# Kernel tuning notes

Measured on AMD Instinct MI355X. Metric: run time of the kernel, lower is better.

## Reference

```python
import jax, jax.numpy as jnp
import numpy as np

B, C, D, H, K = 512, 112, 128, 8, 8  # batch, channels(=seq), d_model, heads, conv kernel
HD = D // H
SCALE = HD ** -0.5
BN_EPS = 1e-5
LN_EPS = 1e-5


def setup_inputs() -> dict:
    key = jax.random.key(0)
    ks = jax.random.split(key, 12)
    s = 0.05
    return {
        "x": jax.random.normal(ks[0], (B, C, D), jnp.float32),
        "conv_w": jax.random.normal(ks[1], (C, 1, K), jnp.float32) * s,
        "conv_b": jax.random.normal(ks[2], (C,), jnp.float32) * s,
        "bn_g": jnp.ones((C,), jnp.float32),
        "bn_b": jnp.zeros((C,), jnp.float32),
        "bn_m": jnp.zeros((C,), jnp.float32),
        "bn_v": jnp.ones((C,), jnp.float32),
        "wq": jax.random.normal(ks[3], (D, D), jnp.float32) * s,
        "bq": jax.random.normal(ks[4], (D,), jnp.float32) * s,
        "wk": jax.random.normal(ks[5], (D, D), jnp.float32) * s,
        "bk": jax.random.normal(ks[6], (D,), jnp.float32) * s,
        "wv": jax.random.normal(ks[7], (D, D), jnp.float32) * s,
        "bv": jax.random.normal(ks[8], (D,), jnp.float32) * s,
        "wo": jax.random.normal(ks[9], (D, D), jnp.float32) * s,
        "bo": jax.random.normal(ks[10], (D,), jnp.float32) * s,
        "ln_g": jnp.ones((D,), jnp.float32),
        "ln_b": jnp.zeros((D,), jnp.float32),
    }


def _forward(x, conv_w, conv_b, bn_g, bn_b, bn_m, bn_v,
             wq, bq, wk, bk, wv, bv, wo, bo, ln_g, ln_b):
    # resnet_1: depthwise Conv1d(padding='same', k=8) -> GELU -> BatchNorm1d (eval)
    # torch 'same' padding for even k: left = (k-1)//2 = 3, right = 4
    h = jax.lax.conv_general_dilated(
        x, conv_w, window_strides=(1,), padding=[(3, 4)],
        dimension_numbers=("NCH", "OIH", "NCH"), feature_group_count=C)
    h = h + conv_b[None, :, None]
    h = jax.nn.gelu(h, approximate=False)
    h = (h - bn_m[None, :, None]) * (bn_g[None, :, None] * jax.lax.rsqrt(bn_v + BN_EPS)[None, :, None]) + bn_b[None, :, None]
    src = x + h  # [B, C, D]; attention treats C as sequence dim

    # multi-head attention (hand-rolled, res_attention path with prev=None)
    q = (src @ wq.T + bq).reshape(B, C, H, HD).transpose(0, 2, 1, 3)  # [B,H,S,hd]
    k = (src @ wk.T + bk).reshape(B, C, H, HD).transpose(0, 2, 1, 3)
    v = (src @ wv.T + bv).reshape(B, C, H, HD).transpose(0, 2, 1, 3)
    scores = jnp.einsum("bhqd,bhkd->bhqk", q, k) * SCALE  # [B,H,S,S]
    attn = jax.nn.softmax(scores, axis=-1)
    out = jnp.einsum("bhqk,bhkd->bhqd", attn, v)  # [B,H,S,hd]
    out = out.transpose(0, 2, 1, 3).reshape(B, C, D)
    out = out @ wo.T + bo

    # residual + LayerNorm over last dim
    src = src + out
    mu = jnp.mean(src, axis=-1, keepdims=True)
    var = jnp.mean(jnp.square(src - mu), axis=-1, keepdims=True)
    src = (src - mu) * jax.lax.rsqrt(var + LN_EPS) * ln_g + ln_b
    return src


def reference(x, conv_w, conv_b, bn_g, bn_b, bn_m, bn_v,
              wq, bq, wk, bk, wv, bv, wo, bo, ln_g, ln_b):
    return _forward(x, conv_w, conv_b, bn_g, bn_b, bn_m, bn_v,
                    wq, bq, wk, bk, wv, bv, wo, bo, ln_g, ln_b)
```

## Files before the change

### kernel.cpp

```cpp
#include <hip/hip_runtime.h>
#include <hip/hip_bf16.h>

#define BB 512
#define CC 112
#define DD 128
#define HH 8
#define HD 16
#define KK 8

typedef unsigned short u16;
typedef short short8 __attribute__((ext_vector_type(8)));
typedef float f32x4 __attribute__((ext_vector_type(4)));

#define MFMA16(a, b, c) __builtin_amdgcn_mfma_f32_16x16x32_bf16(a, b, c, 0, 0, 0)

#define PAD 140

__device__ inline u16 f2bf(float f) {
  union { float f; unsigned u; } v{f};
  unsigned r = (v.u + 0x7FFFu + ((v.u >> 16) & 1u)) >> 16;
  return (u16)r;
}

__global__ __launch_bounds__(128) void k_conv(
    const float* __restrict__ x, const float* __restrict__ cw,
    const float* __restrict__ cb, const float* __restrict__ bg,
    const float* __restrict__ bb_, const float* __restrict__ bm,
    const float* __restrict__ bv, float* __restrict__ src,
    u16* __restrict__ src_b,
    const float* __restrict__ wq, const float* __restrict__ wk,
    const float* __restrict__ wv, const float* __restrict__ wo,
    u16* __restrict__ w_b) {
  const int row = blockIdx.x;
  const int c = row % CC;
  const int d = threadIdx.x;
  __shared__ float sx[DD];
  const size_t base = (size_t)row * DD;
  const float xv = x[base + d];
  sx[d] = xv;
  if (row < 512) {
    const int i = row * 128 + d;
    const int sel = i >> 14, off = i & 16383;
    const float* ws4 = (sel == 0) ? wq : (sel == 1) ? wk : (sel == 2) ? wv : wo;
    w_b[i] = f2bf(ws4[off]);
  }
  __syncthreads();
  float acc = 0.f;
#pragma unroll
  for (int k = 0; k < KK; ++k) {
    const int j = d - 3 + k;
    const float xn = (j >= 0 && j < DD) ? sx[j] : 0.f;
    acc = fmaf(xn, cw[c * KK + k], acc);
  }
  acc += cb[c];
  const float g = 0.5f * acc * (1.f + erff(acc * 0.70710678118654752440f));
  const float h = (g - bm[c]) * (bg[c] * rsqrtf(bv[c] + 1e-5f)) + bb_[c];
  const float s = xv + h;
  src[base + d] = s;
  src_b[base + d] = f2bf(s);
}

__global__ __launch_bounds__(256) void k_qkv(
    const u16* __restrict__ src_b, const u16* __restrict__ w_b,
    const float* __restrict__ bq, const float* __restrict__ bk,
    const float* __restrict__ bv,
    u16* __restrict__ qb, u16* __restrict__ kb, u16* __restrict__ vb) {
  __shared__ u16 sw[128 * PAD];
  const int t = threadIdx.x;
  const int wave = t >> 6, lane = t & 63;
  const int quad = lane >> 4, n = lane & 15;
  const int row0 = blockIdx.x * 64 + wave * 16;

  short8 A[4];
  {
    const size_t rbase = (size_t)(row0 + n) * DD;
#pragma unroll
    for (int kf = 0; kf < 4; ++kf)
      A[kf] = *(const short8*)(src_b + rbase + kf * 32 + quad * 8);
  }
  size_t base_r[4];
#pragma unroll
  for (int r = 0; r < 4; ++r) {
    const int g = row0 + quad * 4 + r;
    const int b_ = g / CC, c_ = g - b_ * CC;
    base_r[r] = ((size_t)b_ * HH * CC + c_) * HD + n;
  }

  const float* const biases[3] = {bq, bk, bv};
  u16* const outs[3] = {qb, kb, vb};
  for (int m = 0; m < 3; ++m) {
    __syncthreads();
    {
      const uint4* wsrc = (const uint4*)(w_b + m * 16384);
      for (int i = t; i < 2048; i += 256) {
        const int r = i >> 4, c = i & 15;
        *(uint4*)&sw[r * PAD + c * 8] = wsrc[r * 16 + c];
      }
    }
    __syncthreads();
    const float* __restrict__ bias = biases[m];
    u16* __restrict__ o = outs[m];
#pragma unroll
    for (int nt = 0; nt < 8; ++nt) {
      f32x4 acc = {0.f, 0.f, 0.f, 0.f};
#pragma unroll
      for (int kf = 0; kf < 4; ++kf) {
        const short8 Bf =
            *(const short8*)&sw[(nt * 16 + n) * PAD + kf * 32 + quad * 8];
        acc = MFMA16(A[kf], Bf, acc);
      }
      const float bcol = bias[nt * 16 + n];
      const size_t hoff = (size_t)nt * CC * HD;
#pragma unroll
      for (int r = 0; r < 4; ++r)
        o[base_r[r] + hoff] = f2bf(acc[r] + bcol);
    }
  }
}

__global__ __launch_bounds__(448) void k_attn(
    const u16* __restrict__ qb_, const u16* __restrict__ kb_,
    const u16* __restrict__ vb_, u16* __restrict__ ab_) {
  const int bh = blockIdx.x;
  const int b = bh >> 3, h = bh & 7;
  const int t = threadIdx.x;
  const int wave = t >> 6;
  const int lane = t & 63;
  const int quad = lane >> 4, n = lane & 15;
  __shared__ u16 VT[HD * PAD];
  __shared__ u16 PL[7 * 16 * PAD];
  const u16* __restrict__ qh = qb_ + (size_t)bh * CC * HD;
  const u16* __restrict__ kh = kb_ + (size_t)bh * CC * HD;
  const u16* __restrict__ vh = vb_ + (size_t)bh * CC * HD;
  u16* __restrict__ aout = ab_ + (size_t)b * CC * DD + h * HD;

  for (int i = t; i < HD * 128; i += 448) {
    const int c = i >> 4, e = i & 15;
    VT[e * PAD + c] = (c < CC) ? vh[c * HD + e] : (u16)0;
  }
  u16* __restrict__ PW = PL + wave * 16 * PAD;
  for (int i = lane; i < 256; i += 64)
    PW[(i >> 4) * PAD + 112 + (i & 15)] = 0;
  __syncthreads();

  const int mt = wave;
  short8 Aq = {};
  if (quad < 2)
    Aq = *(const short8*)(qh + (size_t)(mt * 16 + n) * HD + quad * 8);
  float s[7][4];
#pragma unroll
  for (int jt = 0; jt < 7; ++jt) {
    short8 Bk = {};
    if (quad < 2)
      Bk = *(const short8*)(kh + (size_t)(jt * 16 + n) * HD + quad * 8);
    f32x4 acc = {0.f, 0.f, 0.f, 0.f};
    acc = MFMA16(Aq, Bk, acc);
#pragma unroll
    for (int r = 0; r < 4; ++r) s[jt][r] = acc[r] * 0.25f;
  }
  float mx[4];
#pragma unroll
  for (int r = 0; r < 4; ++r) {
    float m = s[0][r];
#pragma unroll
    for (int jt = 1; jt < 7; ++jt) m = fmaxf(m, s[jt][r]);
    mx[r] = m;
  }
#pragma unroll
  for (int d = 1; d < 16; d <<= 1)
#pragma unroll
    for (int r = 0; r < 4; ++r) mx[r] = fmaxf(mx[r], __shfl_xor(mx[r], d));
  float sm[4] = {0.f, 0.f, 0.f, 0.f};
#pragma unroll
  for (int jt = 0; jt < 7; ++jt)
#pragma unroll
    for (int r = 0; r < 4; ++r) {
      const float p = __expf(s[jt][r] - mx[r]);
      sm[r] += p;
      PW[(quad * 4 + r) * PAD + jt * 16 + n] = f2bf(p);
    }
#pragma unroll
  for (int d = 1; d < 16; d <<= 1)
#pragma unroll
    for (int r = 0; r < 4; ++r) sm[r] += __shfl_xor(sm[r], d);
  __threadfence_block();
  f32x4 o = {0.f, 0.f, 0.f, 0.f};
#pragma unroll
  for (int f = 0; f < 4; ++f) {
    const short8 Ap = *(const short8*)&PW[n * PAD + f * 32 + quad * 8];
    const short8 Bv = *(const short8*)&VT[n * PAD + f * 32 + quad * 8];
    o = MFMA16(Ap, Bv, o);
  }
#pragma unroll
  for (int r = 0; r < 4; ++r) {
    const float val = o[r] * (1.f / sm[r]);
    aout[(size_t)(mt * 16 + quad * 4 + r) * DD + n] = f2bf(val);
  }
}

__global__ __launch_bounds__(256) void k_out(
    const u16* __restrict__ a_b, const u16* __restrict__ w_bo,
    const float* __restrict__ bo, const float* __restrict__ src,
    const float* __restrict__ lg, const float* __restrict__ lb,
    float* __restrict__ out) {
  __shared__ u16 sw[128 * PAD];
  const int t = threadIdx.x;
  const int wave = t >> 6, lane = t & 63;
  const int quad = lane >> 4, n = lane & 15;
  const int row0 = blockIdx.x * 64 + wave * 16;
  {
    const uint4* wsrc = (const uint4*)w_bo;
    for (int i = t; i < 2048; i += 256) {
      const int r = i >> 4, c = i & 15;
      *(uint4*)&sw[r * PAD + c * 8] = wsrc[r * 16 + c];
    }
  }
  short8 A[4];
  {
    const size_t rbase = (size_t)(row0 + n) * DD;
#pragma unroll
    for (int kf = 0; kf < 4; ++kf)
      A[kf] = *(const short8*)(a_b + rbase + kf * 32 + quad * 8);
  }
  __syncthreads();
  float v[8][4];
#pragma unroll
  for (int nt = 0; nt < 8; ++nt) {
    f32x4 acc = {0.f, 0.f, 0.f, 0.f};
#pragma unroll
    for (int kf = 0; kf < 4; ++kf) {
      const short8 Bf =
          *(const short8*)&sw[(nt * 16 + n) * PAD + kf * 32 + quad * 8];
      acc = MFMA16(A[kf], Bf, acc);
    }
    const int col = nt * 16 + n;
    const float bcol = bo[col];
#pragma unroll
    for (int r = 0; r < 4; ++r)
      v[nt][r] = acc[r] + bcol + src[(size_t)(row0 + quad * 4 + r) * DD + col];
  }
  float sum[4] = {0.f, 0.f, 0.f, 0.f}, sq[4] = {0.f, 0.f, 0.f, 0.f};
#pragma unroll
  for (int nt = 0; nt < 8; ++nt)
#pragma unroll
    for (int r = 0; r < 4; ++r) {
      sum[r] += v[nt][r];
      sq[r] = fmaf(v[nt][r], v[nt][r], sq[r]);
    }
#pragma unroll
  for (int d = 1; d < 16; d <<= 1)
#pragma unroll
    for (int r = 0; r < 4; ++r) {
      sum[r] += __shfl_xor(sum[r], d);
      sq[r] += __shfl_xor(sq[r], d);
    }
  float mu[4], rs[4];
#pragma unroll
  for (int r = 0; r < 4; ++r) {
    mu[r] = sum[r] * (1.f / DD);
    const float var = sq[r] * (1.f / DD) - mu[r] * mu[r];
    rs[r] = rsqrtf(var + 1e-5f);
  }
#pragma unroll
  for (int nt = 0; nt < 8; ++nt) {
    const int col = nt * 16 + n;
    const float g = lg[col], be = lb[col];
#pragma unroll
    for (int r = 0; r < 4; ++r)
      out[(size_t)(row0 + quad * 4 + r) * DD + col] =
          (v[nt][r] - mu[r]) * rs[r] * g + be;
  }
}

extern "C" void kernel_launch(void* const* d_in, const int* in_sizes, int n_in,
                              void* d_out, int out_size, void* d_ws,
                              size_t ws_size, hipStream_t stream) {
  (void)in_sizes; (void)n_in; (void)out_size; (void)ws_size;
  const float* x   = (const float*)d_in[0];
  const float* cw  = (const float*)d_in[1];
  const float* cb  = (const float*)d_in[2];
  const float* bg  = (const float*)d_in[3];
  const float* bb  = (const float*)d_in[4];
  const float* bm  = (const float*)d_in[5];
  const float* bv  = (const float*)d_in[6];
  const float* wq  = (const float*)d_in[7];
  const float* bq  = (const float*)d_in[8];
  const float* wk  = (const float*)d_in[9];
  const float* bk  = (const float*)d_in[10];
  const float* wv  = (const float*)d_in[11];
  const float* bvv = (const float*)d_in[12];
  const float* wo  = (const float*)d_in[13];
  const float* bo  = (const float*)d_in[14];
  const float* lg  = (const float*)d_in[15];
  const float* lb  = (const float*)d_in[16];
  float* out = (float*)d_out;

  const size_t NE = (size_t)BB * CC * DD;
  float* s_src = (float*)d_ws;
  u16* ub = (u16*)((char*)d_ws + NE * 4);
  u16* src_b = ub;
  u16* q_b   = ub + NE;
  u16* k_b   = ub + 2 * NE;
  u16* v_b   = ub + 3 * NE;
  u16* a_b   = ub + 4 * NE;
  u16* w_b   = ub + 5 * NE;

  k_conv<<<BB * CC, 128, 0, stream>>>(x, cw, cb, bg, bb, bm, bv, s_src, src_b,
                                      wq, wk, wv, wo, w_b);
  k_qkv<<<(BB * CC) / 64, 256, 0, stream>>>(src_b, w_b, bq, bk, bvv,
                                            q_b, k_b, v_b);
  k_attn<<<BB * HH, 448, 0, stream>>>(q_b, k_b, v_b, a_b);
  k_out<<<(BB * CC) / 64, 256, 0, stream>>>(a_b, w_b + 3 * 16384, bo, s_src,
                                            lg, lb, out);
}
```

Measured before the change: 196.2 us.

## Fuse conv into QKV projection, use 32x32 MFMA attention, drop fp32 src buffer

Merges the depthwise conv/GELU/BN kernel into the QKV projection kernel, computing src directly in registers from x and converting weights to bf16 on the fly. This removes one launch and the fp32 src round trip. V is now written pre-transposed, and attention is rebuilt around 32x32x16 MFMA with 4 waves, exp2-based softmax, and normalization folded into P before the PV product. The output kernel reads the bf16 src for the residual, which lowers residual precision.

```diff
diff --git a/kernel.cpp b/kernel.cpp
--- a/kernel.cpp
+++ b/kernel.cpp
@@ -11,95 +11,113 @@
 typedef unsigned short u16;
 typedef short short8 __attribute__((ext_vector_type(8)));
 typedef float f32x4 __attribute__((ext_vector_type(4)));
+typedef float f32x16 __attribute__((ext_vector_type(16)));
 
 #define MFMA16(a, b, c) __builtin_amdgcn_mfma_f32_16x16x32_bf16(a, b, c, 0, 0, 0)
-
-#define PAD 140
+#define MFMA32(a, b, c) __builtin_amdgcn_mfma_f32_32x32x16_bf16(a, b, c, 0, 0, 0)
+
+#define PAD 136
 
 __device__ inline u16 f2bf(float f) {
   union { float f; unsigned u; } v{f};
   unsigned r = (v.u + 0x7FFFu + ((v.u >> 16) & 1u)) >> 16;
   return (u16)r;
 }
-
-__global__ __launch_bounds__(128) void k_conv(
+__device__ inline float bf2f(u16 u) {
+  union { unsigned u; float f; } v;
+  v.u = ((unsigned)u) << 16;
+  return v.f;
+}
+__device__ inline unsigned pk2(float a, float b) {
+  __hip_bfloat162 h = __float22bfloat162_rn(float2{a, b});
+  union { __hip_bfloat162 h; unsigned u; } v{h};
+  return v.u;
+}
+
+__global__ __launch_bounds__(256) void k_cqkv(
     const float* __restrict__ x, const float* __restrict__ cw,
     const float* __restrict__ cb, const float* __restrict__ bg,
     const float* __restrict__ bb_, const float* __restrict__ bm,
-    const float* __restrict__ bv, float* __restrict__ src,
-    u16* __restrict__ src_b,
-    const float* __restrict__ wq, const float* __restrict__ wk,
-    const float* __restrict__ wv, const float* __restrict__ wo,
-    u16* __restrict__ w_b) {
-  const int row = blockIdx.x;
-  const int c = row % CC;
-  const int d = threadIdx.x;
-  __shared__ float sx[DD];
-  const size_t base = (size_t)row * DD;
-  const float xv = x[base + d];
-  sx[d] = xv;
-  if (row < 512) {
-    const int i = row * 128 + d;
-    const int sel = i >> 14, off = i & 16383;
-    const float* ws4 = (sel == 0) ? wq : (sel == 1) ? wk : (sel == 2) ? wv : wo;
-    w_b[i] = f2bf(ws4[off]);
-  }
-  __syncthreads();
-  float acc = 0.f;
-#pragma unroll
-  for (int k = 0; k < KK; ++k) {
-    const int j = d - 3 + k;
-    const float xn = (j >= 0 && j < DD) ? sx[j] : 0.f;
-    acc = fmaf(xn, cw[c * KK + k], acc);
-  }
-  acc += cb[c];
-  const float g = 0.5f * acc * (1.f + erff(acc * 0.70710678118654752440f));
-  const float h = (g - bm[c]) * (bg[c] * rsqrtf(bv[c] + 1e-5f)) + bb_[c];
-  const float s = xv + h;
-  src[base + d] = s;
-  src_b[base + d] = f2bf(s);
-}
-
-__global__ __launch_bounds__(256) void k_qkv(
-    const u16* __restrict__ src_b, const u16* __restrict__ w_b,
-    const float* __restrict__ bq, const float* __restrict__ bk,
     const float* __restrict__ bv,
-    u16* __restrict__ qb, u16* __restrict__ kb, u16* __restrict__ vb) {
+    const float* __restrict__ wq, const float* __restrict__ bq,
+    const float* __restrict__ wk, const float* __restrict__ bk,
+    const float* __restrict__ wv, const float* __restrict__ bvv,
+    u16* __restrict__ src_b, u16* __restrict__ qb, u16* __restrict__ kb,
+    u16* __restrict__ vtb) {
   __shared__ u16 sw[128 * PAD];
   const int t = threadIdx.x;
   const int wave = t >> 6, lane = t & 63;
   const int quad = lane >> 4, n = lane & 15;
-  const int row0 = blockIdx.x * 64 + wave * 16;
+  const int row_g = blockIdx.x * 64 + wave * 16 + n;
+  const int ch = row_g % CC;
+
+  const float4 w0 = *(const float4*)(cw + ch * KK);
+  const float4 w1 = *(const float4*)(cw + ch * KK + 4);
+  const float cbv = cb[ch];
+  const float bscale = bg[ch] * rsqrtf(bv[ch] + 1e-5f);
+  const float bmv = bm[ch], bbv = bb_[ch];
+
+  const float* __restrict__ xr = x + (size_t)row_g * DD;
+  u16* __restrict__ sbr = src_b + (size_t)row_g * DD;
 
   short8 A[4];
-  {
-    const size_t rbase = (size_t)(row0 + n) * DD;
-#pragma unroll
-    for (int kf = 0; kf < 4; ++kf)
-      A[kf] = *(const short8*)(src_b + rbase + kf * 32 + quad * 8);
-  }
-  size_t base_r[4];
+#pragma unroll
+  for (int kf = 0; kf < 4; ++kf) {
+    const int c0 = kf * 32 + quad * 8;
+    float in[16];
+#pragma unroll
+    for (int f = 0; f < 4; ++f) {
+      const int fi = (c0 >> 2) - 1 + f;
+      float4 vv = {0.f, 0.f, 0.f, 0.f};
+      if (fi >= 0 && fi < 32) vv = ((const float4*)xr)[fi];
+      in[f * 4 + 0] = vv.x; in[f * 4 + 1] = vv.y;
+      in[f * 4 + 2] = vv.z; in[f * 4 + 3] = vv.w;
+    }
+    u16 ob[8];
+#pragma unroll
+    for (int i = 0; i < 8; ++i) {
+      float a = 0.f;
+      a = fmaf(in[i + 1], w0.x, a);
+      a = fmaf(in[i + 2], w0.y, a);
+      a = fmaf(in[i + 3], w0.z, a);
+      a = fmaf(in[i + 4], w0.w, a);
+      a = fmaf(in[i + 5], w1.x, a);
+      a = fmaf(in[i + 6], w1.y, a);
+      a = fmaf(in[i + 7], w1.z, a);
+      a = fmaf(in[i + 8], w1.w, a);
+      a += cbv;
+      const float g = 0.5f * a * (1.f + erff(a * 0.70710678118654752440f));
+      const float s = in[i + 4] + (g - bmv) * bscale + bbv;
+      ob[i] = f2bf(s);
+    }
+    A[kf] = *(short8*)ob;
+    *(short8*)(sbr + c0) = A[kf];
+  }
+
+  const int row0w = blockIdx.x * 64 + wave * 16;
+  int qk_base[4], vt_base[4];
 #pragma unroll
   for (int r = 0; r < 4; ++r) {
-    const int g = row0 + quad * 4 + r;
+    const int g = row0w + quad * 4 + r;
     const int b_ = g / CC, c_ = g - b_ * CC;
-    base_r[r] = ((size_t)b_ * HH * CC + c_) * HD + n;
-  }
-
-  const float* const biases[3] = {bq, bk, bv};
-  u16* const outs[3] = {qb, kb, vb};
+    qk_base[r] = (b_ * (HH * CC) + c_) * HD + n;
+    vt_base[r] = b_ * (HH * HD * CC) + n * CC + c_;
+  }
+
+  const float* const wmats[3] = {wq, wk, wv};
+  const float* const biases[3] = {bq, bk, bvv};
   for (int m = 0; m < 3; ++m) {
     __syncthreads();
     {
-      const uint4* wsrc = (const uint4*)(w_b + m * 16384);
-      for (int i = t; i < 2048; i += 256) {
-        const int r = i >> 4, c = i & 15;
-        *(uint4*)&sw[r * PAD + c * 8] = wsrc[r * 16 + c];
+      const float4* wsrc = (const float4*)wmats[m];
+      for (int i = t; i < 4096; i += 256) {
+        const int r = i >> 5, c4 = (i & 31) * 4;
+        const float4 vv = wsrc[i];
+        *(uint2*)&sw[r * PAD + c4] = uint2{pk2(vv.x, vv.y), pk2(vv.z, vv.w)};
       }
     }
     __syncthreads();
     const float* __restrict__ bias = biases[m];
-    u16* __restrict__ o = outs[m];
 #pragma unroll
     for (int nt = 0; nt < 8; ++nt) {
       f32x4 acc = {0.f, 0.f, 0.f, 0.f};
@@ -110,97 +128,120 @@
         acc = MFMA16(A[kf], Bf, acc);
       }
       const float bcol = bias[nt * 16 + n];
-      const size_t hoff = (size_t)nt * CC * HD;
-#pragma unroll
-      for (int r = 0; r < 4; ++r)
-        o[base_r[r] + hoff] = f2bf(acc[r] + bcol);
-    }
-  }
-}
-
-__global__ __launch_bounds__(448) void k_attn(
+      if (m < 2) {
+        u16* __restrict__ o = (m == 0) ? qb : kb;
+        const int hoff = nt * (CC * HD);
+#pragma unroll
+        for (int r = 0; r < 4; ++r)
+          o[qk_base[r] + hoff] = f2bf(acc[r] + bcol);
+      } else {
+        const int hoff = nt * (HD * CC);
+#pragma unroll
+        for (int r = 0; r < 4; ++r)
+          vtb[vt_base[r] + hoff] = f2bf(acc[r] + bcol);
+      }
+    }
+  }
+}
+
+__global__ __launch_bounds__(256) void k_attn(
     const u16* __restrict__ qb_, const u16* __restrict__ kb_,
-    const u16* __restrict__ vb_, u16* __restrict__ ab_) {
+    const u16* __restrict__ vtb_, u16* __restrict__ ab_) {
   const int bh = blockIdx.x;
   const int b = bh >> 3, h = bh & 7;
   const int t = threadIdx.x;
   const int wave = t >> 6;
   const int lane = t & 63;
-  const int quad = lane >> 4, n = lane & 15;
+  const int lo = lane & 31;
+  const int hi8 = (lane >> 5) * 8;
   __shared__ u16 VT[HD * PAD];
-  __shared__ u16 PL[7 * 16 * PAD];
-  const u16* __restrict__ qh = qb_ + (size_t)bh * CC * HD;
-  const u16* __restrict__ kh = kb_ + (size_t)bh * CC * HD;
-  const u16* __restrict__ vh = vb_ + (size_t)bh * CC * HD;
-  u16* __restrict__ aout = ab_ + (size_t)b * CC * DD + h * HD;
-
-  for (int i = t; i < HD * 128; i += 448) {
-    const int c = i >> 4, e = i & 15;
-    VT[e * PAD + c] = (c < CC) ? vh[c * HD + e] : (u16)0;
-  }
-  u16* __restrict__ PW = PL + wave * 16 * PAD;
-  for (int i = lane; i < 256; i += 64)
-    PW[(i >> 4) * PAD + 112 + (i & 15)] = 0;
+  __shared__ u16 PL[4 * 32 * PAD];
+  const u16* __restrict__ qh = qb_ + (size_t)bh * (CC * HD);
+  const u16* __restrict__ kh = kb_ + (size_t)bh * (CC * HD);
+  const u16* __restrict__ vth = vtb_ + (size_t)bh * (HD * CC);
+  u16* __restrict__ aout = ab_ + (size_t)b * (CC * DD) + h * HD;
+
+  for (int i = t; i < 224; i += 256) {
+    const int e = i / 14, c0 = (i - e * 14) * 8;
+    *(short8*)&VT[e * PAD + c0] = *(const short8*)(vth + e * CC + c0);
+  }
   __syncthreads();
 
-  const int mt = wave;
-  short8 Aq = {};
-  if (quad < 2)
-    Aq = *(const short8*)(qh + (size_t)(mt * 16 + n) * HD + quad * 8);
-  float s[7][4];
-#pragma unroll
-  for (int jt = 0; jt < 7; ++jt) {
-    short8 Bk = {};
-    if (quad < 2)
-      Bk = *(const short8*)(kh + (size_t)(jt * 16 + n) * HD + quad * 8);
-    f32x4 acc = {0.f, 0.f, 0.f, 0.f};
-    acc = MFMA16(Aq, Bk, acc);
-#pragma unroll
-    for (int r = 0; r < 4; ++r) s[jt][r] = acc[r] * 0.25f;
-  }
-  float mx[4];
-#pragma unroll
-  for (int r = 0; r < 4; ++r) {
-    float m = s[0][r];
-#pragma unroll
-    for (int jt = 1; jt < 7; ++jt) m = fmaxf(m, s[jt][r]);
-    mx[r] = m;
-  }
-#pragma unroll
-  for (int d = 1; d < 16; d <<= 1)
-#pragma unroll
-    for (int r = 0; r < 4; ++r) mx[r] = fmaxf(mx[r], __shfl_xor(mx[r], d));
-  float sm[4] = {0.f, 0.f, 0.f, 0.f};
-#pragma unroll
-  for (int jt = 0; jt < 7; ++jt)
-#pragma unroll
-    for (int r = 0; r < 4; ++r) {
-      const float p = __expf(s[jt][r] - mx[r]);
-      sm[r] += p;
-      PW[(quad * 4 + r) * PAD + jt * 16 + n] = f2bf(p);
-    }
-#pragma unroll
-  for (int d = 1; d < 16; d <<= 1)
-#pragma unroll
-    for (int r = 0; r < 4; ++r) sm[r] += __shfl_xor(sm[r], d);
+  u16* __restrict__ PW = PL + wave * (32 * PAD);
+  const int qt0 = wave * 32;
+
+  short8 Bq = {};
+  if (qt0 + lo < CC)
+    Bq = *(const short8*)(qh + (qt0 + lo) * HD + hi8);
+  f32x16 sa[4];
+#pragma unroll
+  for (int mt = 0; mt < 4; ++mt) {
+    short8 Ak = {};
+    const int key = mt * 32 + lo;
+    if (key < CC) Ak = *(const short8*)(kh + key * HD + hi8);
+    f32x16 z = {};
+    sa[mt] = MFMA32(Ak, Bq, z);
+  }
+  const float C1 = 0.25f * 1.44269504088896341f;
+  float mx = -1e30f;
+#pragma unroll
+  for (int mt = 0; mt < 4; ++mt) {
+    const int rmax = (mt == 3) ? 8 : 16;
+#pragma unroll
+    for (int r = 0; r < 16; ++r)
+      if (r < rmax) mx = fmaxf(mx, sa[mt][r]);
+  }
+  mx = fmaxf(mx, __shfl_xor(mx, 32));
+  const float mxc = mx * C1;
+  float sum = 0.f;
+#pragma unroll
+  for (int mt = 0; mt < 4; ++mt) {
+    const int rmax = (mt == 3) ? 8 : 16;
+#pragma unroll
+    for (int r = 0; r < 16; ++r)
+      if (r < rmax) {
+        const float p = exp2f(fmaf(sa[mt][r], C1, -mxc));
+        sa[mt][r] = p;
+        sum += p;
+      }
+  }
+  sum += __shfl_xor(sum, 32);
+  const float rinv = 1.f / sum;
+#pragma unroll
+  for (int mt = 0; mt < 4; ++mt) {
+    const int nruns = (mt == 3) ? 2 : 4;
+#pragma unroll
+    for (int run = 0; run < 4; ++run)
+      if (run < nruns) {
+        const int k0 = mt * 32 + run * 8 + (lane >> 5) * 4;
+        const unsigned u0 =
+            pk2(sa[mt][4 * run + 0] * rinv, sa[mt][4 * run + 1] * rinv);
+        const unsigned u1 =
+            pk2(sa[mt][4 * run + 2] * rinv, sa[mt][4 * run + 3] * rinv);
+        *(uint2*)&PW[lo * PAD + k0] = uint2{u0, u1};
+      }
+  }
   __threadfence_block();
-  f32x4 o = {0.f, 0.f, 0.f, 0.f};
-#pragma unroll
-  for (int f = 0; f < 4; ++f) {
-    const short8 Ap = *(const short8*)&PW[n * PAD + f * 32 + quad * 8];
-    const short8 Bv = *(const short8*)&VT[n * PAD + f * 32 + quad * 8];
-    o = MFMA16(Ap, Bv, o);
-  }
-#pragma unroll
-  for (int r = 0; r < 4; ++r) {
-    const float val = o[r] * (1.f / sm[r]);
-    aout[(size_t)(mt * 16 + quad * 4 + r) * DD + n] = f2bf(val);
+  f32x16 oacc = {};
+#pragma unroll
+  for (int kt = 0; kt < 7; ++kt) {
+    const short8 Ap = *(const short8*)&PW[lo * PAD + kt * 16 + hi8];
+    short8 Bv = {};
+    if (lo < HD) Bv = *(const short8*)&VT[lo * PAD + kt * 16 + hi8];
+    oacc = MFMA32(Ap, Bv, oacc);
+  }
+  if (lo < HD) {
+#pragma unroll
+    for (int r = 0; r < 16; ++r) {
+      const int qrow = qt0 + (r & 3) + 8 * (r >> 2) + 4 * (lane >> 5);
+      if (qrow < CC) aout[(size_t)qrow * DD + lo] = f2bf(oacc[r]);
+    }
   }
 }
 
 __global__ __launch_bounds__(256) void k_out(
-    const u16* __restrict__ a_b, const u16* __restrict__ w_bo,
-    const float* __restrict__ bo, const float* __restrict__ src,
+    const u16* __restrict__ a_b, const float* __restrict__ wo,
+    const float* __restrict__ bo, const u16* __restrict__ src_b,
     const float* __restrict__ lg, const float* __restrict__ lb,
     float* __restrict__ out) {
   __shared__ u16 sw[128 * PAD];
@@ -209,10 +250,11 @@
   const int quad = lane >> 4, n = lane & 15;
   const int row0 = blockIdx.x * 64 + wave * 16;
   {
-    const uint4* wsrc = (const uint4*)w_bo;
-    for (int i = t; i < 2048; i += 256) {
-      const int r = i >> 4, c = i & 15;
-      *(uint4*)&sw[r * PAD + c * 8] = wsrc[r * 16 + c];
+    const float4* wsrc = (const float4*)wo;
+    for (int i = t; i < 4096; i += 256) {
+      const int r = i >> 5, c4 = (i & 31) * 4;
+      const float4 vv = wsrc[i];
+      *(uint2*)&sw[r * PAD + c4] = uint2{pk2(vv.x, vv.y), pk2(vv.z, vv.w)};
     }
   }
   short8 A[4];
@@ -237,7 +279,8 @@
     const float bcol = bo[col];
 #pragma unroll
     for (int r = 0; r < 4; ++r)
-      v[nt][r] = acc[r] + bcol + src[(size_t)(row0 + quad * 4 + r) * DD + col];
+      v[nt][r] = acc[r] + bcol +
+                 bf2f(src_b[(size_t)(row0 + quad * 4 + r) * DD + col]);
   }
   float sum[4] = {0.f, 0.f, 0.f, 0.f}, sq[4] = {0.f, 0.f, 0.f, 0.f};
 #pragma unroll
@@ -296,20 +339,16 @@
   float* out = (float*)d_out;
 
   const size_t NE = (size_t)BB * CC * DD;
-  float* s_src = (float*)d_ws;
-  u16* ub = (u16*)((char*)d_ws + NE * 4);
+  u16* ub = (u16*)d_ws;
   u16* src_b = ub;
   u16* q_b   = ub + NE;
   u16* k_b   = ub + 2 * NE;
-  u16* v_b   = ub + 3 * NE;
+  u16* vt_b  = ub + 3 * NE;
   u16* a_b   = ub + 4 * NE;
-  u16* w_b   = ub + 5 * NE;
-
-  k_conv<<<BB * CC, 128, 0, stream>>>(x, cw, cb, bg, bb, bm, bv, s_src, src_b,
-                                      wq, wk, wv, wo, w_b);
-  k_qkv<<<(BB * CC) / 64, 256, 0, stream>>>(src_b, w_b, bq, bk, bvv,
-                                            q_b, k_b, v_b);
-  k_attn<<<BB * HH, 448, 0, stream>>>(q_b, k_b, v_b, a_b);
-  k_out<<<(BB * CC) / 64, 256, 0, stream>>>(a_b, w_b + 3 * 16384, bo, s_src,
-                                            lg, lb, out);
-}
+
+  k_cqkv<<<(BB * CC) / 64, 256, 0, stream>>>(
+      x, cw, cb, bg, bb, bm, bv, wq, bq, wk, bk, wv, bvv,
+      src_b, q_b, k_b, vt_b);
+  k_attn<<<BB * HH, 256, 0, stream>>>(q_b, k_b, vt_b, a_b);
+  k_out<<<(BB * CC) / 64, 256, 0, stream>>>(a_b, wo, bo, src_b, lg, lb, out);
+}
```

Measured after the change: 186.2 us. -5.1%, faster.
